# Optimization experiments

Measured on AMD Instinct MI355X. Metric: run time of the kernel, lower is better.

## Reference

```python
import jax, jax.numpy as jnp
import numpy as np

K = 16  # neighbors
EPS = 1e-3  # Keras BatchNormalization default epsilon


def _bn(x, gamma, beta, mean, var):
    return (x - mean) * jax.lax.rsqrt(var + EPS) * gamma + beta


def setup_inputs() -> dict:
    key = jax.random.key(0)
    ks = jax.random.split(key, 16)
    B, P, C = 128, 256, 64
    inp = {
        "points": jax.random.normal(ks[0], (B, P, 3), jnp.float32),
        "features": jax.random.normal(ks[1], (B, P, C), jnp.float32),
        "w0": jax.random.normal(ks[2], (2 * C, 64), jnp.float32) * 0.08,
        "w1": jax.random.normal(ks[3], (64, 64), jnp.float32) * 0.12,
        "w2": jax.random.normal(ks[4], (64, 64), jnp.float32) * 0.12,
        "gammas": 0.8 + 0.4 * jax.random.uniform(ks[5], (3, 64), jnp.float32),
        "betas": 0.1 * jax.random.normal(ks[6], (3, 64), jnp.float32),
        "means": 0.1 * jax.random.normal(ks[7], (3, 64), jnp.float32),
        "variances": 0.5 + jax.random.uniform(ks[8], (3, 64), jnp.float32),
        "sc_w": jax.random.normal(ks[9], (C, 64), jnp.float32) * 0.12,
        "sc_gamma": 0.8 + 0.4 * jax.random.uniform(ks[10], (64,), jnp.float32),
        "sc_beta": 0.1 * jax.random.normal(ks[11], (64,), jnp.float32),
        "sc_mean": 0.1 * jax.random.normal(ks[12], (64,), jnp.float32),
        "sc_var": 0.5 + jax.random.uniform(ks[13], (64,), jnp.float32),
    }
    return inp


def reference(points, features, w0, w1, w2, gammas, betas, means, variances,
              sc_w, sc_gamma, sc_beta, sc_mean, sc_var):
    B, P, C = features.shape
    # pairwise squared-distance matrix: ||a||^2 - 2 a.b + ||b||^2  -> [B, P, P]
    r = jnp.sum(points * points, axis=2, keepdims=True)  # [B, P, 1]
    m = jnp.einsum('bpc,bqc->bpq', points, points)
    d = r - 2.0 * m + jnp.swapaxes(r, 1, 2)
    # top_k of -d: K+1 nearest (incl. self at position 0), drop self
    _, idx = jax.lax.top_k(-d, K + 1)
    idx = idx[:, :, 1:]  # [B, P, K]
    # KNN gather of features
    knn_fts = features[jnp.arange(B)[:, None, None], idx]  # [B, P, K, C]
    center = jnp.broadcast_to(features[:, :, None, :], (B, P, K, C))
    x = jnp.concatenate([center, knn_fts - center], axis=-1)  # [B, P, K, 2C]
    # per-edge MLP: 1x1 conv + BN (inference) + relu
    for i, w in enumerate((w0, w1, w2)):
        x = jnp.einsum('bpkc,cd->bpkd', x, w)
        x = _bn(x, gammas[i], betas[i], means[i], variances[i])
        x = jax.nn.relu(x)
    fts = jnp.mean(x, axis=2)  # average pooling over neighbors -> [B, P, 64]
    # shortcut 1x1 conv + BN
    sc = jnp.einsum('bpc,cd->bpd', features, sc_w)
    sc = _bn(sc, sc_gamma, sc_beta, sc_mean, sc_var)
    return jax.nn.relu(sc + fts)
```

## Files before the change

### kernel.cpp

```cpp
#include <hip/hip_runtime.h>
#include <math.h>

#define NBATCH 128
#define NP 256
#define NC 64
#define KNN 16
#define EPSV 1e-3f

typedef __bf16 bf16_t;
typedef bf16_t bf16x8 __attribute__((ext_vector_type(8)));
typedef float f32x4 __attribute__((ext_vector_type(4)));
typedef unsigned short u16x4 __attribute__((ext_vector_type(4)));

static __device__ __forceinline__ f32x4 mfma16(bf16x8 a, bf16x8 b, f32x4 c) {
    return __builtin_amdgcn_mfma_f32_16x16x32_bf16(a, b, c, 0, 0, 0);
}
static __device__ __forceinline__ unsigned short f2bfu(float f) {
    union { bf16_t b; unsigned short u; } cv; cv.b = (bf16_t)f; return cv.u;
}
static __device__ __forceinline__ unsigned umin2(unsigned a, unsigned b) { return a < b ? a : b; }
static __device__ __forceinline__ unsigned umax2(unsigned a, unsigned b) { return a > b ? a : b; }

#define CFENCE() asm volatile("" ::: "memory")

#define INSERTK(k_)                                                   \
    do {                                                              \
        _Pragma("unroll")                                             \
        for (int ii = KNN - 1; ii >= 1; --ii)                         \
            bk[ii] = umin2(umax2((k_), bk[ii - 1]), bk[ii]);          \
        bk[0] = umin2((k_), bk[0]);                                   \
    } while (0)

__global__ __launch_bounds__(256) void setup_kernel(
    const float* __restrict__ points, const float* __restrict__ features,
    const float* __restrict__ w0, const float* __restrict__ w1,
    const float* __restrict__ w2, const float* __restrict__ sc_w,
    const float* __restrict__ gammas, const float* __restrict__ betas,
    const float* __restrict__ means, const float* __restrict__ variances,
    const float* __restrict__ sc_gamma, const float* __restrict__ sc_beta,
    const float* __restrict__ sc_mean, const float* __restrict__ sc_var,
    unsigned short* __restrict__ fbf, unsigned short* __restrict__ wsf,
    float* __restrict__ bnp, int* __restrict__ knn_out)
{
    const int bid = blockIdx.x;
    if (bid < 1024) {
        const int tid = bid * 256 + threadIdx.x;
        const float4 a = ((const float4*)features)[tid * 2];
        const float4 b = ((const float4*)features)[tid * 2 + 1];
        union { unsigned short s[8]; uint4 v; } r;
        r.s[0] = f2bfu(a.x); r.s[1] = f2bfu(a.y); r.s[2] = f2bfu(a.z); r.s[3] = f2bfu(a.w);
        r.s[4] = f2bfu(b.x); r.s[5] = f2bfu(b.y); r.s[6] = f2bfu(b.z); r.s[7] = f2bfu(b.w);
        ((uint4*)fbf)[tid] = r.v;
    } else if (bid < 1105) {
        const int tid = (bid - 1024) * 256 + threadIdx.x;
        if (tid < 20480) {
            const int region = tid >> 12;
            const int e2 = tid & 4095;
            const int f = e2 >> 9;
            const int r = e2 & 511;
            const int lane = r >> 3, j = r & 7;
            const int ks = f >> 2, t = f & 3;
            const int row = ks * 32 + (lane >> 4) * 8 + j;
            const int col = 4 * (lane & 15) + t;
            float v;
            if (region == 0)      v = w0[row * 64 + col] - w0[(64 + row) * 64 + col];
            else if (region == 1) v = w0[(64 + row) * 64 + col];
            else if (region == 2) v = w1[row * 64 + col];
            else if (region == 3) v = w2[row * 64 + col];
            else                  v = sc_w[row * 64 + col];
            wsf[tid] = f2bfu(v);
        } else {
            const int e = tid - 20480;
            if (e < 192) {
                float s = gammas[e] * rsqrtf(variances[e] + EPSV);
                bnp[e] = s;
                bnp[192 + e] = betas[e] - means[e] * s;
            } else if (e < 256) {
                const int d = e - 192;
                float s = sc_gamma[d] * rsqrtf(sc_var[d] + EPSV);
                bnp[384 + d] = s;
                bnp[448 + d] = sc_beta[d] - sc_mean[d] * s;
            }
        }
    } else {
        __shared__ __align__(16) float4 sp[NP];
        __shared__ unsigned sk[128][17];
        const int kb = bid - 1105;
        const int bb = kb >> 1;
        const int qbase = (kb & 1) * 128;
        const int t = threadIdx.x;
        const int qt = t & 127;
        const int half = t >> 7;
        const int p = qbase + qt;

        const float* pb = points + (size_t)bb * NP * 3;
        sp[t] = make_float4(pb[t * 3 + 0], pb[t * 3 + 1], pb[t * 3 + 2], 0.f);
        __syncthreads();

        const float4 qp = sp[p];
        unsigned bk[KNN];
#pragma unroll
        for (int i = 0; i < KNN; ++i) bk[i] = 0xFFFFFFFFu;

        const int cbase = half * 128;
#pragma unroll 4
        for (int c = 0; c < 128; ++c) {
            const int cand = cbase + c;
            const float4 P = sp[cand];
            const float dx = qp.x - P.x, dy = qp.y - P.y, dz = qp.z - P.z;
            const float d = fmaf(dx, dx, fmaf(dy, dy, dz * dz));
            unsigned key = (__float_as_uint(d) & 0xFFFFFF00u) | (unsigned)cand;
            key = (cand == p) ? 0xFFFFFFFFu : key;
            INSERTK(key);
        }

        if (half == 1) {
#pragma unroll
            for (int i = 0; i < KNN; ++i) sk[qt][i] = bk[i];
        }
        __syncthreads();
        if (half == 0) {
            for (int j = 0; j < KNN; ++j) {
                const unsigned key = sk[qt][j];
                if (key >= bk[KNN - 1]) break;
                INSERTK(key);
            }
            int* op = knn_out + ((size_t)bb * NP + p) * KNN;
#pragma unroll
            for (int i = 0; i < KNN; ++i) op[i] = (int)(bk[i] & 0xFFu);
        }
    }
}

__global__ __launch_bounds__(256) void edge_kernel(
    const unsigned short* __restrict__ fbf, const int* __restrict__ knn_idx,
    const unsigned short* __restrict__ wsf, const float* __restrict__ bnp,
    float* __restrict__ out)
{
    __shared__ __align__(16) unsigned short slab[4][2][16 * 72];
    __shared__ __align__(16) float s0buf[4][8][64];
    __shared__ __align__(16) float ftsbuf[4][8][64];

    const int tid = threadIdx.x;
    const int wid = tid >> 6;
    const int l = tid & 63;
    const int i = l & 15;
    const int h = l >> 4;
    const int wg = (blockIdx.x & 7) * 128 + (blockIdx.x >> 3);
    const int p0 = (wg * 4 + wid) * 8;
    const int b = p0 >> 8;

    unsigned short* sl0 = slab[wid][0];
    unsigned short* sl1 = slab[wid][1];

    const bf16x8* __restrict__ WV = (const bf16x8*)(wsf);
    const bf16x8* __restrict__ W0H = (const bf16x8*)(wsf + 4096);
    const bf16x8* __restrict__ W1 = (const bf16x8*)(wsf + 8192);
    const bf16x8* __restrict__ W2 = (const bf16x8*)(wsf + 12288);

    bf16x8 w0h[2][4], w1r[2][4], w2r[2][4];
#pragma unroll
    for (int ks = 0; ks < 2; ++ks)
#pragma unroll
        for (int t = 0; t < 4; ++t) {
            w0h[ks][t] = W0H[(ks * 4 + t) * 64 + l];
            w1r[ks][t] = W1[(ks * 4 + t) * 64 + l];
            w2r[ks][t] = W2[(ks * 4 + t) * 64 + l];
        }

    float4 scl[3], shf[3];
#pragma unroll
    for (int L = 0; L < 3; ++L) {
        scl[L] = *(const float4*)&bnp[L * 64 + 4 * i];
        shf[L] = *(const float4*)&bnp[192 + L * 64 + 4 * i];
    }

    {
        const unsigned short* cp = fbf + (size_t)(p0 + (i & 7)) * NC;
        bf16x8 a0 = *(const bf16x8*)(cp + 8 * h);
        bf16x8 a1 = *(const bf16x8*)(cp + 32 + 8 * h);
        f32x4 acc[4];
#pragma unroll
        for (int t = 0; t < 4; ++t) {
            f32x4 z = {0.f, 0.f, 0.f, 0.f};
            z = mfma16(a0, WV[t * 64 + l], z);
            acc[t] = mfma16(a1, WV[(4 + t) * 64 + l], z);
        }
        if (h < 2) {
#pragma unroll
            for (int r = 0; r < 4; ++r) {
                float4 v = make_float4(acc[0][r], acc[1][r], acc[2][r], acc[3][r]);
                *(float4*)&s0buf[wid][h * 4 + r][4 * i] = v;
            }
        }
    }
    int nks[8];
#pragma unroll
    for (int q = 0; q < 8; ++q) nks[q] = knn_idx[(size_t)(p0 + q) * KNN + i];
    CFENCE();

#pragma unroll
    for (int qp = 0; qp < 4; ++qp) {
        const int q0 = 2 * qp, q1 = 2 * qp + 1;
        bf16x8 f00, f01, f10, f11;
        {
            const unsigned short* sp0 = fbf + (size_t)(b * NP + nks[q0]) * NC;
            const unsigned short* sp1 = fbf + (size_t)(b * NP + nks[q1]) * NC;
            f00 = *(const bf16x8*)(sp0 + 8 * h);
            f01 = *(const bf16x8*)(sp0 + 32 + 8 * h);
            f10 = *(const bf16x8*)(sp1 + 8 * h);
            f11 = *(const bf16x8*)(sp1 + 32 + 8 * h);
        }
        {
            float4 s0a = *(const float4*)&s0buf[wid][q0][4 * i];
            const float* sc_ = (const float*)&scl[0];
            const float* sh_ = (const float*)&shf[0];
            f32x4 acc[4];
#pragma unroll
            for (int t = 0; t < 4; ++t) {
                f32x4 z = {0.f, 0.f, 0.f, 0.f};
                z = mfma16(f00, w0h[0][t], z);
                acc[t] = mfma16(f01, w0h[1][t], z);
            }
            const float* sp_ = (const float*)&s0a;
#pragma unroll
            for (int r = 0; r < 4; ++r) {
                u16x4 pk;
#pragma unroll
                for (int t = 0; t < 4; ++t)
                    pk[t] = f2bfu(fmaxf(fmaf(acc[t][r] + sp_[t], sc_[t], sh_[t]), 0.f));
                *(u16x4*)&sl0[(h * 4 + r) * 72 + 4 * i] = pk;
            }
            float4 s0b = *(const float4*)&s0buf[wid][q1][4 * i];
            const float* sq_ = (const float*)&s0b;
#pragma unroll
            for (int t = 0; t < 4; ++t) {
                f32x4 z = {0.f, 0.f, 0.f, 0.f};
                z = mfma16(f10, w0h[0][t], z);
                acc[t] = mfma16(f11, w0h[1][t], z);
            }
#pragma unroll
            for (int r = 0; r < 4; ++r) {
                u16x4 pk;
#pragma unroll
                for (int t = 0; t < 4; ++t)
                    pk[t] = f2bfu(fmaxf(fmaf(acc[t][r] + sq_[t], sc_[t], sh_[t]), 0.f));
                *(u16x4*)&sl1[(h * 4 + r) * 72 + 4 * i] = pk;
            }
        }
        CFENCE();

        {
            bf16x8 xa0 = *(const bf16x8*)(sl0 + i * 72 + h * 8);
            bf16x8 xa1 = *(const bf16x8*)(sl0 + i * 72 + h * 8 + 32);
            bf16x8 xb0 = *(const bf16x8*)(sl1 + i * 72 + h * 8);
            bf16x8 xb1 = *(const bf16x8*)(sl1 + i * 72 + h * 8 + 32);
            const float* sc_ = (const float*)&scl[1];
            const float* sh_ = (const float*)&shf[1];
            f32x4 acc[4];
#pragma unroll
            for (int t = 0; t < 4; ++t) {
                f32x4 z = {0.f, 0.f, 0.f, 0.f};
                z = mfma16(xa0, w1r[0][t], z);
                acc[t] = mfma16(xa1, w1r[1][t], z);
            }
#pragma unroll
            for (int r = 0; r < 4; ++r) {
                u16x4 pk;
#pragma unroll
                for (int t = 0; t < 4; ++t)
                    pk[t] = f2bfu(fmaxf(fmaf(acc[t][r], sc_[t], sh_[t]), 0.f));
                *(u16x4*)&sl0[(h * 4 + r) * 72 + 4 * i] = pk;
            }
#pragma unroll
            for (int t = 0; t < 4; ++t) {
                f32x4 z = {0.f, 0.f, 0.f, 0.f};
                z = mfma16(xb0, w1r[0][t], z);
                acc[t] = mfma16(xb1, w1r[1][t], z);
            }
#pragma unroll
            for (int r = 0; r < 4; ++r) {
                u16x4 pk;
#pragma unroll
                for (int t = 0; t < 4; ++t)
                    pk[t] = f2bfu(fmaxf(fmaf(acc[t][r], sc_[t], sh_[t]), 0.f));
                *(u16x4*)&sl1[(h * 4 + r) * 72 + 4 * i] = pk;
            }
        }
        CFENCE();

        {
            bf16x8 xa0 = *(const bf16x8*)(sl0 + i * 72 + h * 8);
            bf16x8 xa1 = *(const bf16x8*)(sl0 + i * 72 + h * 8 + 32);
            bf16x8 xb0 = *(const bf16x8*)(sl1 + i * 72 + h * 8);
            bf16x8 xb1 = *(const bf16x8*)(sl1 + i * 72 + h * 8 + 32);
            const float* sc_ = (const float*)&scl[2];
            const float* sh_ = (const float*)&shf[2];
            float sa[4], sb[4];
#pragma unroll
            for (int t = 0; t < 4; ++t) {
                f32x4 z = {0.f, 0.f, 0.f, 0.f};
                z = mfma16(xa0, w2r[0][t], z);
                f32x4 acc = mfma16(xa1, w2r[1][t], z);
                float s = 0.f;
#pragma unroll
                for (int r = 0; r < 4; ++r)
                    s += fmaxf(fmaf(acc[r], sc_[t], sh_[t]), 0.f);
                z = (f32x4){0.f, 0.f, 0.f, 0.f};
                z = mfma16(xb0, w2r[0][t], z);
                f32x4 accb = mfma16(xb1, w2r[1][t], z);
                float sB = 0.f;
#pragma unroll
                for (int r = 0; r < 4; ++r)
                    sB += fmaxf(fmaf(accb[r], sc_[t], sh_[t]), 0.f);
                s += __shfl_xor(s, 16, 64);
                s += __shfl_xor(s, 32, 64);
                sB += __shfl_xor(sB, 16, 64);
                sB += __shfl_xor(sB, 32, 64);
                sa[t] = s * (1.f / 16.f);
                sb[t] = sB * (1.f / 16.f);
            }
            if (h == 0) {
                *(float4*)&ftsbuf[wid][q0][4 * i] = make_float4(sa[0], sa[1], sa[2], sa[3]);
                *(float4*)&ftsbuf[wid][q1][4 * i] = make_float4(sb[0], sb[1], sb[2], sb[3]);
            }
        }
        CFENCE();
    }

    {
        const bf16x8* __restrict__ WS = (const bf16x8*)(wsf + 16384);
        float4 sscl = *(const float4*)&bnp[384 + 4 * i];
        float4 sshf = *(const float4*)&bnp[448 + 4 * i];
        const unsigned short* fp = fbf + (size_t)(p0 + (i & 7)) * NC;
        bf16x8 a0 = *(const bf16x8*)(fp + 8 * h);
        bf16x8 a1 = *(const bf16x8*)(fp + 32 + 8 * h);
        f32x4 acc[4];
#pragma unroll
        for (int t = 0; t < 4; ++t) {
            f32x4 z = {0.f, 0.f, 0.f, 0.f};
            z = mfma16(a0, WS[t * 64 + l], z);
            acc[t] = mfma16(a1, WS[(4 + t) * 64 + l], z);
        }
        if (h < 2) {
            const float* ss_ = (const float*)&sscl;
            const float* sf_ = (const float*)&sshf;
#pragma unroll
            for (int r = 0; r < 4; ++r) {
                const int q = h * 4 + r;
                float4 fts = *(const float4*)&ftsbuf[wid][q][4 * i];
                const float* ft_ = (const float*)&fts;
                float4 o;
                float* o_ = (float*)&o;
#pragma unroll
                for (int t = 0; t < 4; ++t)
                    o_[t] = fmaxf(fmaf(acc[t][r], ss_[t], sf_[t]) + ft_[t], 0.f);
                *(float4*)&out[(size_t)(p0 + q) * NC + 4 * i] = o;
            }
        }
    }
}

extern "C" void kernel_launch(void* const* d_in, const int* in_sizes, int n_in,
                              void* d_out, int out_size, void* d_ws, size_t ws_size,
                              hipStream_t stream) {
    const float* points    = (const float*)d_in[0];
    const float* features  = (const float*)d_in[1];
    const float* w0        = (const float*)d_in[2];
    const float* w1        = (const float*)d_in[3];
    const float* w2        = (const float*)d_in[4];
    const float* gammas    = (const float*)d_in[5];
    const float* betas     = (const float*)d_in[6];
    const float* means     = (const float*)d_in[7];
    const float* variances = (const float*)d_in[8];
    const float* sc_w      = (const float*)d_in[9];
    const float* sc_gamma  = (const float*)d_in[10];
    const float* sc_beta   = (const float*)d_in[11];
    const float* sc_mean   = (const float*)d_in[12];
    const float* sc_var    = (const float*)d_in[13];
    float* out = (float*)d_out;

    int* knn_buf = (int*)d_ws;
    unsigned short* fbf = (unsigned short*)((char*)d_ws + (1 << 21));
    unsigned short* wsf = (unsigned short*)((char*)d_ws + (3 << 21));
    float* bnp = (float*)((char*)d_ws + (3 << 21) + 40960);

    setup_kernel<<<1361, 256, 0, stream>>>(points, features, w0, w1, w2, sc_w,
                                           gammas, betas, means, variances,
                                           sc_gamma, sc_beta, sc_mean, sc_var,
                                           fbf, wsf, bnp, knn_buf);
    edge_kernel<<<NBATCH * NP / 32, 256, 0, stream>>>(fbf, knn_buf, wsf, bnp, out);
}
```

Before: 48.40 us.

## Stage MLP weights in LDS, prefetch neighbor rows, shuffle center term

Moves the three per-edge weight matrices out of per-lane registers into a shared LDS copy loaded cooperatively by the block, which frees many VGPRs and may raise occupancy. The center-feature term is now passed between lanes with ds_bpermute instead of going through a shared scratch buffer. Neighbor feature rows for the next pair are prefetched one step ahead, and the A/B MFMA chains are interleaved. In exchange it adds a block-wide barrier, extra LDS reads of the weights on every iteration, and higher LDS usage per block.

```diff
diff --git a/kernel.cpp b/kernel.cpp
--- a/kernel.cpp
+++ b/kernel.cpp
@@ -20,6 +20,9 @@
 }
 static __device__ __forceinline__ unsigned umin2(unsigned a, unsigned b) { return a < b ? a : b; }
 static __device__ __forceinline__ unsigned umax2(unsigned a, unsigned b) { return a > b ? a : b; }
+static __device__ __forceinline__ float bperm_f32(int idx, float v) {
+    return __int_as_float(__builtin_amdgcn_ds_bpermute(idx, __float_as_int(v)));
+}
 
 #define CFENCE() asm volatile("" ::: "memory")
 
@@ -137,8 +140,8 @@
     const unsigned short* __restrict__ wsf, const float* __restrict__ bnp,
     float* __restrict__ out)
 {
+    __shared__ __align__(16) unsigned short wlds[24 * 512];
     __shared__ __align__(16) unsigned short slab[4][2][16 * 72];
-    __shared__ __align__(16) float s0buf[4][8][64];
     __shared__ __align__(16) float ftsbuf[4][8][64];
 
     const int tid = threadIdx.x;
@@ -153,20 +156,13 @@
     unsigned short* sl0 = slab[wid][0];
     unsigned short* sl1 = slab[wid][1];
 
-    const bf16x8* __restrict__ WV = (const bf16x8*)(wsf);
-    const bf16x8* __restrict__ W0H = (const bf16x8*)(wsf + 4096);
-    const bf16x8* __restrict__ W1 = (const bf16x8*)(wsf + 8192);
-    const bf16x8* __restrict__ W2 = (const bf16x8*)(wsf + 12288);
-
-    bf16x8 w0h[2][4], w1r[2][4], w2r[2][4];
-#pragma unroll
-    for (int ks = 0; ks < 2; ++ks)
-#pragma unroll
-        for (int t = 0; t < 4; ++t) {
-            w0h[ks][t] = W0H[(ks * 4 + t) * 64 + l];
-            w1r[ks][t] = W1[(ks * 4 + t) * 64 + l];
-            w2r[ks][t] = W2[(ks * 4 + t) * 64 + l];
-        }
+    {
+        const uint4* src = (const uint4*)(wsf + 4096);
+        uint4* dst = (uint4*)wlds;
+#pragma unroll
+        for (int k = 0; k < 6; ++k) dst[tid + k * 256] = src[tid + k * 256];
+    }
+    #define WF(fi_) (*(const bf16x8*)&wlds[(fi_) * 512 + l * 8])
 
     float4 scl[3], shf[3];
 #pragma unroll
@@ -175,78 +171,83 @@
         shf[L] = *(const float4*)&bnp[192 + L * 64 + 4 * i];
     }
 
+    f32x4 s0acc[4];
     {
+        const bf16x8* __restrict__ WV = (const bf16x8*)(wsf);
         const unsigned short* cp = fbf + (size_t)(p0 + (i & 7)) * NC;
         bf16x8 a0 = *(const bf16x8*)(cp + 8 * h);
         bf16x8 a1 = *(const bf16x8*)(cp + 32 + 8 * h);
-        f32x4 acc[4];
 #pragma unroll
         for (int t = 0; t < 4; ++t) {
             f32x4 z = {0.f, 0.f, 0.f, 0.f};
             z = mfma16(a0, WV[t * 64 + l], z);
-            acc[t] = mfma16(a1, WV[(4 + t) * 64 + l], z);
-        }
-        if (h < 2) {
-#pragma unroll
-            for (int r = 0; r < 4; ++r) {
-                float4 v = make_float4(acc[0][r], acc[1][r], acc[2][r], acc[3][r]);
-                *(float4*)&s0buf[wid][h * 4 + r][4 * i] = v;
-            }
+            s0acc[t] = mfma16(a1, WV[(4 + t) * 64 + l], z);
         }
     }
     int nks[8];
 #pragma unroll
     for (int q = 0; q < 8; ++q) nks[q] = knn_idx[(size_t)(p0 + q) * KNN + i];
-    CFENCE();
+
+    __syncthreads();
+
+    const int i4 = 4 * i;
+
+    bf16x8 f00, f01, f10, f11;
+    {
+        const unsigned short* sp0 = fbf + (size_t)(b * NP + nks[0]) * NC;
+        const unsigned short* sp1 = fbf + (size_t)(b * NP + nks[1]) * NC;
+        f00 = *(const bf16x8*)(sp0 + 8 * h);
+        f01 = *(const bf16x8*)(sp0 + 32 + 8 * h);
+        f10 = *(const bf16x8*)(sp1 + 8 * h);
+        f11 = *(const bf16x8*)(sp1 + 32 + 8 * h);
+    }
 
 #pragma unroll
     for (int qp = 0; qp < 4; ++qp) {
         const int q0 = 2 * qp, q1 = 2 * qp + 1;
-        bf16x8 f00, f01, f10, f11;
+        const int idxp = (qp >> 1) * 64 + i4;
+        float s0a[4], s0b[4];
+#pragma unroll
+        for (int t = 0; t < 4; ++t) {
+            s0a[t] = bperm_f32(idxp, s0acc[t][q0 & 3]);
+            s0b[t] = bperm_f32(idxp, s0acc[t][q1 & 3]);
+        }
+
         {
-            const unsigned short* sp0 = fbf + (size_t)(b * NP + nks[q0]) * NC;
-            const unsigned short* sp1 = fbf + (size_t)(b * NP + nks[q1]) * NC;
-            f00 = *(const bf16x8*)(sp0 + 8 * h);
-            f01 = *(const bf16x8*)(sp0 + 32 + 8 * h);
-            f10 = *(const bf16x8*)(sp1 + 8 * h);
-            f11 = *(const bf16x8*)(sp1 + 32 + 8 * h);
-        }
-        {
-            float4 s0a = *(const float4*)&s0buf[wid][q0][4 * i];
+            f32x4 accA[4], accB[4];
+#pragma unroll
+            for (int t = 0; t < 4; ++t) {
+                bf16x8 wt0 = WF(t);
+                bf16x8 wt1 = WF(4 + t);
+                f32x4 z = {0.f, 0.f, 0.f, 0.f};
+                z = mfma16(f00, wt0, z);
+                accA[t] = mfma16(f01, wt1, z);
+                z = (f32x4){0.f, 0.f, 0.f, 0.f};
+                z = mfma16(f10, wt0, z);
+                accB[t] = mfma16(f11, wt1, z);
+            }
             const float* sc_ = (const float*)&scl[0];
             const float* sh_ = (const float*)&shf[0];
-            f32x4 acc[4];
-#pragma unroll
-            for (int t = 0; t < 4; ++t) {
-                f32x4 z = {0.f, 0.f, 0.f, 0.f};
-                z = mfma16(f00, w0h[0][t], z);
-                acc[t] = mfma16(f01, w0h[1][t], z);
-            }
-            const float* sp_ = (const float*)&s0a;
 #pragma unroll
             for (int r = 0; r < 4; ++r) {
-                u16x4 pk;
-#pragma unroll
-                for (int t = 0; t < 4; ++t)
-                    pk[t] = f2bfu(fmaxf(fmaf(acc[t][r] + sp_[t], sc_[t], sh_[t]), 0.f));
-                *(u16x4*)&sl0[(h * 4 + r) * 72 + 4 * i] = pk;
-            }
-            float4 s0b = *(const float4*)&s0buf[wid][q1][4 * i];
-            const float* sq_ = (const float*)&s0b;
-#pragma unroll
-            for (int t = 0; t < 4; ++t) {
-                f32x4 z = {0.f, 0.f, 0.f, 0.f};
-                z = mfma16(f10, w0h[0][t], z);
-                acc[t] = mfma16(f11, w0h[1][t], z);
-            }
-#pragma unroll
-            for (int r = 0; r < 4; ++r) {
-                u16x4 pk;
-#pragma unroll
-                for (int t = 0; t < 4; ++t)
-                    pk[t] = f2bfu(fmaxf(fmaf(acc[t][r] + sq_[t], sc_[t], sh_[t]), 0.f));
-                *(u16x4*)&sl1[(h * 4 + r) * 72 + 4 * i] = pk;
-            }
+                u16x4 pkA, pkB;
+#pragma unroll
+                for (int t = 0; t < 4; ++t) {
+                    pkA[t] = f2bfu(fmaxf(fmaf(accA[t][r] + s0a[t], sc_[t], sh_[t]), 0.f));
+                    pkB[t] = f2bfu(fmaxf(fmaf(accB[t][r] + s0b[t], sc_[t], sh_[t]), 0.f));
+                }
+                *(u16x4*)&sl0[(h * 4 + r) * 72 + i4] = pkA;
+                *(u16x4*)&sl1[(h * 4 + r) * 72 + i4] = pkB;
+            }
+        }
+        bf16x8 g00, g01, g10, g11;
+        if (qp < 3) {
+            const unsigned short* sp0 = fbf + (size_t)(b * NP + nks[(q0 + 2) & 7]) * NC;
+            const unsigned short* sp1 = fbf + (size_t)(b * NP + nks[(q1 + 2) & 7]) * NC;
+            g00 = *(const bf16x8*)(sp0 + 8 * h);
+            g01 = *(const bf16x8*)(sp0 + 32 + 8 * h);
+            g10 = *(const bf16x8*)(sp1 + 8 * h);
+            g11 = *(const bf16x8*)(sp1 + 32 + 8 * h);
         }
         CFENCE();
 
@@ -255,36 +256,30 @@
             bf16x8 xa1 = *(const bf16x8*)(sl0 + i * 72 + h * 8 + 32);
             bf16x8 xb0 = *(const bf16x8*)(sl1 + i * 72 + h * 8);
             bf16x8 xb1 = *(const bf16x8*)(sl1 + i * 72 + h * 8 + 32);
+            f32x4 accA[4], accB[4];
+#pragma unroll
+            for (int t = 0; t < 4; ++t) {
+                bf16x8 wt0 = WF(8 + t);
+                bf16x8 wt1 = WF(12 + t);
+                f32x4 z = {0.f, 0.f, 0.f, 0.f};
+                z = mfma16(xa0, wt0, z);
+                accA[t] = mfma16(xa1, wt1, z);
+                z = (f32x4){0.f, 0.f, 0.f, 0.f};
+                z = mfma16(xb0, wt0, z);
+                accB[t] = mfma16(xb1, wt1, z);
+            }
             const float* sc_ = (const float*)&scl[1];
             const float* sh_ = (const float*)&shf[1];
-            f32x4 acc[4];
-#pragma unroll
-            for (int t = 0; t < 4; ++t) {
-                f32x4 z = {0.f, 0.f, 0.f, 0.f};
-                z = mfma16(xa0, w1r[0][t], z);
-                acc[t] = mfma16(xa1, w1r[1][t], z);
-            }
 #pragma unroll
             for (int r = 0; r < 4; ++r) {
-                u16x4 pk;
-#pragma unroll
-                for (int t = 0; t < 4; ++t)
-                    pk[t] = f2bfu(fmaxf(fmaf(acc[t][r], sc_[t], sh_[t]), 0.f));
-                *(u16x4*)&sl0[(h * 4 + r) * 72 + 4 * i] = pk;
-            }
-#pragma unroll
-            for (int t = 0; t < 4; ++t) {
-                f32x4 z = {0.f, 0.f, 0.f, 0.f};
-                z = mfma16(xb0, w1r[0][t], z);
-                acc[t] = mfma16(xb1, w1r[1][t], z);
-            }
-#pragma unroll
-            for (int r = 0; r < 4; ++r) {
-                u16x4 pk;
-#pragma unroll
-                for (int t = 0; t < 4; ++t)
-                    pk[t] = f2bfu(fmaxf(fmaf(acc[t][r], sc_[t], sh_[t]), 0.f));
-                *(u16x4*)&sl1[(h * 4 + r) * 72 + 4 * i] = pk;
+                u16x4 pkA, pkB;
+#pragma unroll
+                for (int t = 0; t < 4; ++t) {
+                    pkA[t] = f2bfu(fmaxf(fmaf(accA[t][r], sc_[t], sh_[t]), 0.f));
+                    pkB[t] = f2bfu(fmaxf(fmaf(accB[t][r], sc_[t], sh_[t]), 0.f));
+                }
+                *(u16x4*)&sl0[(h * 4 + r) * 72 + i4] = pkA;
+                *(u16x4*)&sl1[(h * 4 + r) * 72 + i4] = pkB;
             }
         }
         CFENCE();
@@ -299,20 +294,20 @@
             float sa[4], sb[4];
 #pragma unroll
             for (int t = 0; t < 4; ++t) {
+                bf16x8 wt0 = WF(16 + t);
+                bf16x8 wt1 = WF(20 + t);
                 f32x4 z = {0.f, 0.f, 0.f, 0.f};
-                z = mfma16(xa0, w2r[0][t], z);
-                f32x4 acc = mfma16(xa1, w2r[1][t], z);
-                float s = 0.f;
-#pragma unroll
-                for (int r = 0; r < 4; ++r)
-                    s += fmaxf(fmaf(acc[r], sc_[t], sh_[t]), 0.f);
+                z = mfma16(xa0, wt0, z);
+                f32x4 accA = mfma16(xa1, wt1, z);
                 z = (f32x4){0.f, 0.f, 0.f, 0.f};
-                z = mfma16(xb0, w2r[0][t], z);
-                f32x4 accb = mfma16(xb1, w2r[1][t], z);
-                float sB = 0.f;
-#pragma unroll
-                for (int r = 0; r < 4; ++r)
-                    sB += fmaxf(fmaf(accb[r], sc_[t], sh_[t]), 0.f);
+                z = mfma16(xb0, wt0, z);
+                f32x4 accB = mfma16(xb1, wt1, z);
+                float s = 0.f, sB = 0.f;
+#pragma unroll
+                for (int r = 0; r < 4; ++r) {
+                    s += fmaxf(fmaf(accA[r], sc_[t], sh_[t]), 0.f);
+                    sB += fmaxf(fmaf(accB[r], sc_[t], sh_[t]), 0.f);
+                }
                 s += __shfl_xor(s, 16, 64);
                 s += __shfl_xor(s, 32, 64);
                 sB += __shfl_xor(sB, 16, 64);
@@ -321,17 +316,18 @@
                 sb[t] = sB * (1.f / 16.f);
             }
             if (h == 0) {
-                *(float4*)&ftsbuf[wid][q0][4 * i] = make_float4(sa[0], sa[1], sa[2], sa[3]);
-                *(float4*)&ftsbuf[wid][q1][4 * i] = make_float4(sb[0], sb[1], sb[2], sb[3]);
+                *(float4*)&ftsbuf[wid][q0][i4] = make_float4(sa[0], sa[1], sa[2], sa[3]);
+                *(float4*)&ftsbuf[wid][q1][i4] = make_float4(sb[0], sb[1], sb[2], sb[3]);
             }
         }
         CFENCE();
+        f00 = g00; f01 = g01; f10 = g10; f11 = g11;
     }
 
     {
         const bf16x8* __restrict__ WS = (const bf16x8*)(wsf + 16384);
-        float4 sscl = *(const float4*)&bnp[384 + 4 * i];
-        float4 sshf = *(const float4*)&bnp[448 + 4 * i];
+        float4 sscl = *(const float4*)&bnp[384 + i4];
+        float4 sshf = *(const float4*)&bnp[448 + i4];
         const unsigned short* fp = fbf + (size_t)(p0 + (i & 7)) * NC;
         bf16x8 a0 = *(const bf16x8*)(fp + 8 * h);
         bf16x8 a1 = *(const bf16x8*)(fp + 32 + 8 * h);
@@ -348,17 +344,18 @@
 #pragma unroll
             for (int r = 0; r < 4; ++r) {
                 const int q = h * 4 + r;
-                float4 fts = *(const float4*)&ftsbuf[wid][q][4 * i];
+                float4 fts = *(const float4*)&ftsbuf[wid][q][i4];
                 const float* ft_ = (const float*)&fts;
                 float4 o;
                 float* o_ = (float*)&o;
 #pragma unroll
                 for (int t = 0; t < 4; ++t)
                     o_[t] = fmaxf(fmaf(acc[t][r], ss_[t], sf_[t]) + ft_[t], 0.f);
-                *(float4*)&out[(size_t)(p0 + q) * NC + 4 * i] = o;
-            }
-        }
-    }
+                *(float4*)&out[(size_t)(p0 + q) * NC + i4] = o;
+            }
+        }
+    }
+    #undef WF
 }
 
 extern "C" void kernel_launch(void* const* d_in, const int* in_sizes, int n_in,
```

After: 46.64 us. -3.6%, faster.
